# Optimization experiments

Measured on AMD Instinct MI355X. Metric: run time of the kernel, lower is better.

The kernel has to match this reference:

```python
import jax, jax.numpy as jnp
import numpy as np

N = 50000      # nodes
E = 800000     # edges
IN = 128       # in_dim
EMB = 32       # emb_dim
ED = 8         # edge_dim
L = 4          # num_layers
B = 64         # num graphs in batch
OUT = 10       # out_dim
EPS = 1e-5


def setup_inputs() -> dict:
    key = jax.random.key(0)
    ks = jax.random.split(key, 16)
    f32 = jnp.float32
    def nrm(k, shape, scale):
        return jax.random.normal(k, shape, dtype=f32) * scale
    inp = {}
    inp['x'] = nrm(ks[0], (N, IN), 1.0)
    inp['edge_index'] = jax.random.randint(ks[1], (2, E), 0, N)
    inp['edge_attr'] = nrm(ks[2], (E, ED), 1.0)
    inp['batch'] = jnp.sort(jax.random.randint(ks[3], (N,), 0, B))
    # lin_in
    inp['lin_in_w'] = nrm(ks[4], (IN, EMB), 0.05)
    inp['lin_in_b'] = jnp.zeros((EMB,), f32)
    # per-layer message MLP: Linear(2e+ed->e), BN, ReLU, Linear(e->e), BN, ReLU
    inp['msg_w1'] = nrm(ks[5], (L, 2 * EMB + ED, EMB), 0.1)
    inp['msg_b1'] = jnp.zeros((L, EMB), f32)
    inp['msg_g1'] = jnp.ones((L, EMB), f32)
    inp['msg_be1'] = jnp.zeros((L, EMB), f32)
    inp['msg_w2'] = nrm(ks[6], (L, EMB, EMB), 0.1)
    inp['msg_b2'] = jnp.zeros((L, EMB), f32)
    inp['msg_g2'] = jnp.ones((L, EMB), f32)
    inp['msg_be2'] = jnp.zeros((L, EMB), f32)
    # per-layer update MLP: Linear(2e->e), BN, ReLU, Linear(e->e), BN, ReLU
    inp['upd_w1'] = nrm(ks[7], (L, 2 * EMB, EMB), 0.1)
    inp['upd_b1'] = jnp.zeros((L, EMB), f32)
    inp['upd_g1'] = jnp.ones((L, EMB), f32)
    inp['upd_be1'] = jnp.zeros((L, EMB), f32)
    inp['upd_w2'] = nrm(ks[8], (L, EMB, EMB), 0.1)
    inp['upd_b2'] = jnp.zeros((L, EMB), f32)
    inp['upd_g2'] = jnp.ones((L, EMB), f32)
    inp['upd_be2'] = jnp.zeros((L, EMB), f32)
    # lin_pred
    inp['pred_w'] = nrm(ks[9], (EMB, OUT), 0.1)
    inp['pred_b'] = jnp.zeros((OUT,), f32)
    return inp


def _bn(x, g, b):
    # BatchNorm1d in training mode: batch stats over dim 0 (biased variance)
    mu = jnp.mean(x, axis=0)
    var = jnp.mean(jnp.square(x - mu), axis=0)
    return (x - mu) * jax.lax.rsqrt(var + EPS) * g + b


def reference(x, edge_attr, lin_in_w, lin_in_b,
              msg_w1, msg_b1, msg_g1, msg_be1, msg_w2, msg_b2, msg_g2, msg_be2,
              upd_w1, upd_b1, upd_g1, upd_be1, upd_w2, upd_b2, upd_g2, upd_be2,
              pred_w, pred_b, edge_index, batch):
    src = edge_index[0]  # h_j source nodes
    dst = edge_index[1]  # h_i target nodes (aggregation index)
    h = x @ lin_in_w + lin_in_b  # [N, EMB]
    for i in range(L):
        # message: gather + concat + MLP(BN,ReLU)x2 over edges
        msg_in = jnp.concatenate([h[dst], h[src], edge_attr], axis=-1)  # [E, 2e+ed]
        m = jax.nn.relu(_bn(msg_in @ msg_w1[i] + msg_b1[i], msg_g1[i], msg_be1[i]))
        m = jax.nn.relu(_bn(m @ msg_w2[i] + msg_b2[i], msg_g2[i], msg_be2[i]))
        # aggregate: scatter-add by destination
        aggr = jax.ops.segment_sum(m, dst, num_segments=N)  # [N, EMB]
        # update: concat + MLP(BN,ReLU)x2
        u = jnp.concatenate([h, aggr], axis=-1)  # [N, 2e]
        u = jax.nn.relu(_bn(u @ upd_w1[i] + upd_b1[i], upd_g1[i], upd_be1[i]))
        u = jax.nn.relu(_bn(u @ upd_w2[i] + upd_b2[i], upd_g2[i], upd_be2[i]))
        h = u + h  # residual in MPNNModel.get_embeddings
    # global mean pool
    sums = jax.ops.segment_sum(h, batch, num_segments=B)
    counts = jax.ops.segment_sum(jnp.ones((N,), h.dtype), batch, num_segments=B)
    h_graph = sums / jnp.maximum(counts, 1.0)[:, None]
    return h_graph @ pred_w + pred_b  # [B, OUT]
```

## Files before the change

kernel.cpp:

```cpp
#include <hip/hip_runtime.h>
#include <cstddef>

#define N_NODES 50000
#define N_EDGES 800000
#define IN_DIM  128
#define EMB     32
#define ED      8
#define NLAYERS 4
#define NB      64
#define OUTD    10
#define EPS_BN  1e-5f

#define EDGE_GRID 3125
#define NODE_GRID 196
#define NODE4_GRID 782
#define AU_GRID   6250
#define MSG1_EPT  2
#define MSG1_GRID 1563
#define NT16      50000
#define NTILE_N   3125
#define LIN_GRID  782
#define MSG2_TPW  16
#define MSG2_GRID 782

#define SREP 4

typedef short bf16x8 __attribute__((ext_vector_type(8)));
typedef float f32x4  __attribute__((ext_vector_type(4)));


__device__ __forceinline__ unsigned short f2bf(float x) {
  union { float f; unsigned u; } v; v.f = x;
  unsigned b = v.u + 0x7FFFu + ((v.u >> 16) & 1u);
  return (unsigned short)(b >> 16);
}
__device__ __forceinline__ float bf2f(unsigned short s) {
  union { unsigned u; float f; } v; v.u = ((unsigned)s) << 16;
  return v.f;
}

__device__ __forceinline__ void coef_from_stats(const float* __restrict__ stats_stage,
                                                const float* __restrict__ g,
                                                const float* __restrict__ be,
                                                float inv_count, float* __restrict__ cf) {
  if (threadIdx.x < EMB) {
    const int c = threadIdx.x;
    float s = 0.f, ss = 0.f;
#pragma unroll
    for (int r = 0; r < SREP; ++r) {
      s  += stats_stage[r*64 + c];
      ss += stats_stage[r*64 + EMB + c];
    }
    const float mu  = s * inv_count;
    const float var = ss * inv_count - mu*mu;
    const float a = g[c] * rsqrtf(var + EPS_BN);
    cf[c] = a;
    cf[EMB + c] = fmaf(-mu, a, be[c]);
  }
  __syncthreads();
}

__device__ __forceinline__ void block_stats_atomic(const float ts[EMB], const float tss[EMB],
                                                   float* __restrict__ stats_stage) {
  __shared__ float sred[256];
  const int lane = threadIdx.x & 63;
  const int wid  = threadIdx.x >> 6;
#pragma unroll
  for (int c = 0; c < EMB; ++c) {
    float a = ts[c];
    float q = tss[c];
#pragma unroll
    for (int o = 32; o > 0; o >>= 1) {
      a += __shfl_down(a, o, 64);
      q += __shfl_down(q, o, 64);
    }
    if (lane == 0) { sred[wid*64 + c] = a; sred[wid*64 + EMB + c] = q; }
  }
  __syncthreads();
  if (threadIdx.x < 64) {
    const float v = sred[threadIdx.x] + sred[64 + threadIdx.x] +
                    sred[128 + threadIdx.x] + sred[192 + threadIdx.x];
    atomicAdd(stats_stage + ((blockIdx.x & (SREP-1)) << 6) + threadIdx.x, v);
  }
}

__device__ __forceinline__ void wave_stats_atomic(float ts[8], float tss[8],
                                                  float* __restrict__ lds_s,
                                                  float* __restrict__ lds_q,
                                                  float* __restrict__ stats_stage) {
  const int lane = threadIdx.x & 63;
  const int wv   = threadIdx.x >> 6;
#pragma unroll
  for (int j = 0; j < 8; ++j) {
    float a = ts[j], b = tss[j];
#pragma unroll
    for (int o = 32; o > 0; o >>= 1) {
      a += __shfl_down(a, o, 64);
      b += __shfl_down(b, o, 64);
    }
    ts[j] = a; tss[j] = b;
  }
  if (lane == 0) {
#pragma unroll
    for (int j = 0; j < 8; ++j) {
      lds_s[wv*8 + j] = ts[j];
      lds_q[wv*8 + j] = tss[j];
    }
  }
  __syncthreads();
  if (threadIdx.x < 64) {
    const float v = (threadIdx.x < 32) ? lds_s[threadIdx.x] : lds_q[threadIdx.x - 32];
    atomicAdd(stats_stage + ((blockIdx.x & (SREP-1)) << 6) + threadIdx.x, v);
  }
}

__device__ __forceinline__ void mac8_f4(float acc[8], const float4 v, const float* wk) {
#pragma unroll
  for (int j = 0; j < 8; ++j) acc[j] = fmaf(v.x, wk[j], acc[j]);
#pragma unroll
  for (int j = 0; j < 8; ++j) acc[j] = fmaf(v.y, wk[EMB + j], acc[j]);
#pragma unroll
  for (int j = 0; j < 8; ++j) acc[j] = fmaf(v.z, wk[2*EMB + j], acc[j]);
#pragma unroll
  for (int j = 0; j < 8; ++j) acc[j] = fmaf(v.w, wk[3*EMB + j], acc[j]);
}

#define HSTRIDE 40

__global__ __launch_bounds__(256) void k_lin_in_pq(
    const float* __restrict__ x, const float* __restrict__ w, const float* __restrict__ b,
    const float* __restrict__ w1, const float* __restrict__ b1, const int* __restrict__ ei,
    float* __restrict__ h, unsigned short* __restrict__ p, unsigned short* __restrict__ q,
    int* __restrict__ cnt)
{
  __shared__ __align__(16) unsigned short lds_hb[4][16*HSTRIDE];
  __shared__ __align__(16) unsigned short lds_pq[4][16*HSTRIDE];
  const int lane = threadIdx.x & 63;
  const int wv   = threadIdx.x >> 6;
  const int n0i  = lane & 15;
  const int quad = lane >> 4;

  const int tile = blockIdx.x*4 + wv;
  if (tile < NTILE_N) {
    const int r0 = tile*16;
    bf16x8 BwL[4], BwH[4];
#pragma unroll
    for (int kb = 0; kb < 4; ++kb) {
#pragma unroll
      for (int j = 0; j < 8; ++j) {
        const int k = kb*32 + quad*8 + j;
        BwL[kb][j] = (short)f2bf(w[k*EMB + n0i]);
        BwH[kb][j] = (short)f2bf(w[k*EMB + 16 + n0i]);
      }
    }
    f32x4 accL = {0.f,0.f,0.f,0.f};
    f32x4 accH = {0.f,0.f,0.f,0.f};
#pragma unroll
    for (int kb = 0; kb < 4; ++kb) {
      const float4 xa = *(const float4*)(x + (size_t)(r0 + n0i)*IN_DIM + kb*32 + quad*8);
      const float4 xb = *(const float4*)(x + (size_t)(r0 + n0i)*IN_DIM + kb*32 + quad*8 + 4);
      bf16x8 A;
      A[0] = (short)f2bf(xa.x); A[1] = (short)f2bf(xa.y);
      A[2] = (short)f2bf(xa.z); A[3] = (short)f2bf(xa.w);
      A[4] = (short)f2bf(xb.x); A[5] = (short)f2bf(xb.y);
      A[6] = (short)f2bf(xb.z); A[7] = (short)f2bf(xb.w);
      accL = __builtin_amdgcn_mfma_f32_16x16x32_bf16(A, BwL[kb], accL, 0, 0, 0);
      accH = __builtin_amdgcn_mfma_f32_16x16x32_bf16(A, BwH[kb], accH, 0, 0, 0);
    }
    const float bL = b[n0i], bH = b[16 + n0i];
#pragma unroll
    for (int r = 0; r < 4; ++r) {
      const int row = quad*4 + r;
      const float vL = accL[r] + bL;
      const float vH = accH[r] + bH;
      h[(size_t)(r0 + row)*EMB + n0i]      = vL;
      h[(size_t)(r0 + row)*EMB + 16 + n0i] = vH;
      lds_hb[wv][row*HSTRIDE + n0i]      = f2bf(vL);
      lds_hb[wv][row*HSTRIDE + 16 + n0i] = f2bf(vH);
    }
    bf16x8 A2;
#pragma unroll
    for (int j = 0; j < 8; ++j)
      A2[j] = (short)lds_hb[wv][n0i*HSTRIDE + quad*8 + j];
    bf16x8 BpL, BpH, BqL, BqH;
#pragma unroll
    for (int j = 0; j < 8; ++j) {
      const int k = quad*8 + j;
      BpL[j] = (short)f2bf(w1[k*EMB + n0i]);
      BpH[j] = (short)f2bf(w1[k*EMB + 16 + n0i]);
      BqL[j] = (short)f2bf(w1[(EMB + k)*EMB + n0i]);
      BqH[j] = (short)f2bf(w1[(EMB + k)*EMB + 16 + n0i]);
    }
    const f32x4 z4 = {0.f,0.f,0.f,0.f};
    f32x4 pL = __builtin_amdgcn_mfma_f32_16x16x32_bf16(A2, BpL, z4, 0, 0, 0);
    f32x4 pH = __builtin_amdgcn_mfma_f32_16x16x32_bf16(A2, BpH, z4, 0, 0, 0);
    f32x4 qL = __builtin_amdgcn_mfma_f32_16x16x32_bf16(A2, BqL, z4, 0, 0, 0);
    f32x4 qH = __builtin_amdgcn_mfma_f32_16x16x32_bf16(A2, BqH, z4, 0, 0, 0);
    const float b1L = b1[n0i], b1H = b1[16 + n0i];
#pragma unroll
    for (int r = 0; r < 4; ++r) {
      const int row = quad*4 + r;
      lds_pq[wv][row*HSTRIDE + n0i]      = f2bf(pL[r] + b1L);
      lds_pq[wv][row*HSTRIDE + 16 + n0i] = f2bf(pH[r] + b1H);
    }
    {
      const int row2 = lane >> 2;
      const int c8   = (lane & 3)*8;
      const uint4 ov = *(const uint4*)&lds_pq[wv][row2*HSTRIDE + c8];
      *(uint4*)(p + (size_t)(r0 + row2)*EMB + c8) = ov;
    }
#pragma unroll
    for (int r = 0; r < 4; ++r) {
      const int row = quad*4 + r;
      lds_pq[wv][row*HSTRIDE + n0i]      = f2bf(qL[r]);
      lds_pq[wv][row*HSTRIDE + 16 + n0i] = f2bf(qH[r]);
    }
    {
      const int row2 = lane >> 2;
      const int c8   = (lane & 3)*8;
      const uint4 ov = *(const uint4*)&lds_pq[wv][row2*HSTRIDE + c8];
      *(uint4*)(q + (size_t)(r0 + row2)*EMB + c8) = ov;
    }
  }
  for (int e = blockIdx.x*256 + threadIdx.x; e < N_EDGES; e += gridDim.x*256)
    atomicAdd(&cnt[ei[N_EDGES + e]], 1);
}

__global__ __launch_bounds__(256) void k_scan_a(const int* __restrict__ cnt,
                                                int* __restrict__ row_ptr, int* __restrict__ bsum) {
  __shared__ int s[256];
  const int gid = blockIdx.x*256 + threadIdx.x;
  const int v = (gid < N_NODES) ? cnt[gid] : 0;
  s[threadIdx.x] = v;
  __syncthreads();
  for (int o = 1; o < 256; o <<= 1) {
    const int t = (threadIdx.x >= o) ? s[threadIdx.x - o] : 0;
    __syncthreads();
    s[threadIdx.x] += t;
    __syncthreads();
  }
  if (gid < N_NODES) row_ptr[gid] = s[threadIdx.x] - v;
  if (threadIdx.x == 255) bsum[blockIdx.x] = s[255];
}

__global__ __launch_bounds__(256) void k_scan_bc(int* __restrict__ row_ptr,
                                                 const int* __restrict__ bsum) {
  __shared__ int s[256];
  const int t = threadIdx.x;
  const int v = (t < NODE_GRID) ? bsum[t] : 0;
  s[t] = v;
  __syncthreads();
  for (int o = 1; o < 256; o <<= 1) {
    const int tt = (t >= o) ? s[t - o] : 0;
    __syncthreads();
    s[t] += tt;
    __syncthreads();
  }
  const int off = (blockIdx.x == 0) ? 0 : s[blockIdx.x - 1];
  const int gid = blockIdx.x*256 + t;
  if (gid < N_NODES) row_ptr[gid] += off;
  if (blockIdx.x == 0 && t == 0) row_ptr[N_NODES] = N_EDGES;
}

__global__ __launch_bounds__(256) void k_place_scatter(
    const int* __restrict__ ei, const float* __restrict__ ea,
    const int* __restrict__ row_ptr, int* __restrict__ cnt2,
    int* __restrict__ src_perm, int* __restrict__ dst_perm,
    unsigned short* __restrict__ ea_perm)
{
  const int e = blockIdx.x*256 + threadIdx.x;
  const int d = ei[N_EDGES + e];
  const int pos = row_ptr[d] + atomicAdd(&cnt2[d], 1);
  src_perm[pos] = ei[e];
  dst_perm[pos] = d;
  const float4 v0 = ((const float4*)(ea + (size_t)e*ED))[0];
  const float4 v1 = ((const float4*)(ea + (size_t)e*ED))[1];
  const float ev[8] = {v0.x, v0.y, v0.z, v0.w, v1.x, v1.y, v1.z, v1.w};
  unsigned u[4];
#pragma unroll
  for (int j = 0; j < 4; ++j)
    u[j] = (unsigned)f2bf(ev[2*j]) | ((unsigned)f2bf(ev[2*j+1]) << 16);
  uint4 o; o.x = u[0]; o.y = u[1]; o.z = u[2]; o.w = u[3];
  *(uint4*)(ea_perm + (size_t)pos*ED) = o;
}


__global__ __launch_bounds__(256) void k_msg1(
    const unsigned short* __restrict__ pb, const unsigned short* __restrict__ qb,
    const int* __restrict__ src_perm, const int* __restrict__ dst_perm,
    const unsigned short* __restrict__ ea_perm,
    const float* __restrict__ w1b,
    unsigned short* __restrict__ y, float* __restrict__ stats)
{
  float ts[EMB], tss[EMB];
#pragma unroll
  for (int c = 0; c < EMB; ++c) { ts[c] = 0.f; tss[c] = 0.f; }
  const int base = blockIdx.x*(256*MSG1_EPT) + threadIdx.x;
  for (int it = 0; it < MSG1_EPT; ++it) {
    const int i = base + it*256;
    if (i >= N_EDGES) break;
    const int dst = dst_perm[i];
    const int src = src_perm[i];
    float acc[EMB];
    const uint4* pd = (const uint4*)(pb + (size_t)dst*EMB);
    const uint4* qs = (const uint4*)(qb + (size_t)src*EMB);
#pragma unroll
    for (int j4 = 0; j4 < 4; ++j4) {
      const uint4 a = pd[j4];
      const uint4 b = qs[j4];
      const unsigned ua[4] = {a.x, a.y, a.z, a.w};
      const unsigned ub[4] = {b.x, b.y, b.z, b.w};
#pragma unroll
      for (int t = 0; t < 4; ++t) {
        acc[j4*8 + 2*t]   = bf2f((unsigned short)(ua[t] & 0xFFFFu)) +
                            bf2f((unsigned short)(ub[t] & 0xFFFFu));
        acc[j4*8 + 2*t+1] = bf2f((unsigned short)(ua[t] >> 16)) +
                            bf2f((unsigned short)(ub[t] >> 16));
      }
    }
    const uint4 eraw = *(const uint4*)(ea_perm + (size_t)i*ED);
    const unsigned ue[4] = {eraw.x, eraw.y, eraw.z, eraw.w};
    float ev[8];
#pragma unroll
    for (int t = 0; t < 4; ++t) {
      ev[2*t]   = bf2f((unsigned short)(ue[t] & 0xFFFFu));
      ev[2*t+1] = bf2f((unsigned short)(ue[t] >> 16));
    }
#pragma unroll
    for (int k = 0; k < 8; ++k) {
      const float* wk = w1b + k*EMB;
#pragma unroll
      for (int c = 0; c < EMB; ++c) acc[c] = fmaf(ev[k], wk[c], acc[c]);
    }
    unsigned short us[EMB];
#pragma unroll
    for (int c = 0; c < EMB; ++c) us[c] = f2bf(acc[c]);
    unsigned u[16];
#pragma unroll
    for (int j = 0; j < 16; ++j)
      u[j] = (unsigned)us[2*j] | ((unsigned)us[2*j+1] << 16);
    uint4* dp = (uint4*)(y + (size_t)i*EMB);
#pragma unroll
    for (int j = 0; j < 4; ++j) {
      uint4 o; o.x = u[4*j]; o.y = u[4*j+1]; o.z = u[4*j+2]; o.w = u[4*j+3];
      dp[j] = o;
    }
#pragma unroll
    for (int c = 0; c < EMB; ++c) {
      const float v = bf2f(us[c]);
      ts[c] += v;
      tss[c] = fmaf(v, v, tss[c]);
    }
  }
  block_stats_atomic(ts, tss, stats);
}

__global__ __launch_bounds__(256) void k_msg2(
    unsigned short* __restrict__ y,
    const float* __restrict__ stats1, const float* __restrict__ g1, const float* __restrict__ be1,
    const float* __restrict__ w2, const float* __restrict__ b2,
    float* __restrict__ stats2)
{
  __shared__ __align__(16) unsigned short lds_t[4][16*32];
  __shared__ float lds_s[4][32], lds_q[4][32];
  __shared__ float cf[64];

  coef_from_stats(stats1, g1, be1, 1.0f/(float)N_EDGES, cf);

  const int lane = threadIdx.x & 63;
  const int wid  = threadIdx.x >> 6;
  const int n0 = lane & 15;
  const int kb = lane >> 4;

  bf16x8 Blo, Bhi;
#pragma unroll
  for (int j = 0; j < 8; ++j) {
    Blo[j] = (short)f2bf(w2[(kb*8 + j)*EMB + n0]);
    Bhi[j] = (short)f2bf(w2[(kb*8 + j)*EMB + 16 + n0]);
  }
  float a1[8], c1[8];
#pragma unroll
  for (int j = 0; j < 8; ++j) {
    a1[j] = cf[kb*8 + j];
    c1[j] = cf[EMB + kb*8 + j];
  }
  const float b2c0 = b2[n0], b2c1 = b2[16 + n0];

  float ts[8], tss[8];
#pragma unroll
  for (int j = 0; j < 8; ++j) { ts[j] = 0.f; tss[j] = 0.f; }

  const int tile0 = blockIdx.x * (MSG2_TPW*4);
  for (int t = 0; t < MSG2_TPW; ++t) {
    const int tile = tile0 + t*4 + wid;
    if (tile >= NT16) break;
    const size_t e0 = (size_t)tile * 16;

    const uint4 araw = *(const uint4*)(y + (e0 + n0)*EMB + kb*8);
    unsigned int ua[4] = {araw.x, araw.y, araw.z, araw.w};
    bf16x8 A;
#pragma unroll
    for (int j = 0; j < 4; ++j) {
      float v0 = bf2f((unsigned short)(ua[j] & 0xFFFFu));
      float v1 = bf2f((unsigned short)(ua[j] >> 16));
      v0 = fmaxf(fmaf(a1[2*j],   v0, c1[2*j]),   0.f);
      v1 = fmaxf(fmaf(a1[2*j+1], v1, c1[2*j+1]), 0.f);
      A[2*j]   = (short)f2bf(v0);
      A[2*j+1] = (short)f2bf(v1);
    }

    f32x4 acc0 = {0.f, 0.f, 0.f, 0.f};
    f32x4 acc1 = {0.f, 0.f, 0.f, 0.f};
    acc0 = __builtin_amdgcn_mfma_f32_16x16x32_bf16(A, Blo, acc0, 0, 0, 0);
    acc1 = __builtin_amdgcn_mfma_f32_16x16x32_bf16(A, Bhi, acc1, 0, 0, 0);

#pragma unroll
    for (int r = 0; r < 4; ++r) {
      const int row = kb*4 + r;
      lds_t[wid][row*32 + n0]      = f2bf(acc0[r] + b2c0);
      lds_t[wid][row*32 + 16 + n0] = f2bf(acc1[r] + b2c1);
    }
    const uint4 orow = *(const uint4*)&lds_t[wid][(lane>>2)*32 + (lane&3)*8];
    *(uint4*)(y + (e0 + (lane>>2))*EMB + (lane&3)*8) = orow;

    unsigned int uo[4] = {orow.x, orow.y, orow.z, orow.w};
#pragma unroll
    for (int j = 0; j < 4; ++j) {
      const float v0 = bf2f((unsigned short)(uo[j] & 0xFFFFu));
      const float v1 = bf2f((unsigned short)(uo[j] >> 16));
      ts[2*j]   += v0;  tss[2*j]   = fmaf(v0, v0, tss[2*j]);
      ts[2*j+1] += v1;  tss[2*j+1] = fmaf(v1, v1, tss[2*j+1]);
    }
  }

#pragma unroll
  for (int j = 0; j < 8; ++j) {
    float s = ts[j], qq = tss[j];
#pragma unroll
    for (int o = 4; o < 64; o <<= 1) {
      s  += __shfl_xor(s, o, 64);
      qq += __shfl_xor(qq, o, 64);
    }
    ts[j] = s; tss[j] = qq;
  }
  if (lane < 4) {
#pragma unroll
    for (int j = 0; j < 8; ++j) {
      lds_s[wid][lane*8 + j] = ts[j];
      lds_q[wid][lane*8 + j] = tss[j];
    }
  }
  __syncthreads();
  if (threadIdx.x < 64) {
    const int c = threadIdx.x & 31;
    const int kind = threadIdx.x >> 5;
    float v = 0.f;
#pragma unroll
    for (int wq = 0; wq < 4; ++wq)
      v += kind ? lds_q[wq][c] : lds_s[wq][c];
    atomicAdd(stats2 + ((blockIdx.x & (SREP-1)) << 6) + kind*32 + c, v);
  }
}

__global__ __launch_bounds__(256) void k_aggr_upd1(
    const unsigned short* __restrict__ y, const int* __restrict__ row_ptr,
    const float* __restrict__ h,
    const float* __restrict__ stats1, const float* __restrict__ g2, const float* __restrict__ be2,
    const float* __restrict__ uw1, const float* __restrict__ ub1,
    float* __restrict__ z, float* __restrict__ stats2)
{
  __shared__ float cf[64];
  __shared__ float lh[8][32];
  __shared__ float la[8][32];
  __shared__ float rs[4][32], rq[4][32];
  coef_from_stats(stats1, g2, be2, 1.0f/(float)N_EDGES, cf);

  const int g = threadIdx.x >> 5;
  const int l = threadIdx.x & 31;
  const int n = blockIdx.x*8 + g;

  lh[g][l] = h[(size_t)n*EMB + l];

  const int rof = l >> 4;
  const int cp  = l & 15;
  const float a0 = cf[2*cp],     b0 = cf[EMB + 2*cp];
  const float a1 = cf[2*cp + 1], b1 = cf[EMB + 2*cp + 1];
  const int lo = row_ptr[n], hi = row_ptr[n+1];
  float s0 = 0.f, s1 = 0.f;
  for (int i = lo + rof; i < hi; i += 2) {
    const unsigned u = *(const unsigned*)(y + (size_t)i*EMB + 2*cp);
    const float v0 = bf2f((unsigned short)(u & 0xFFFFu));
    const float v1 = bf2f((unsigned short)(u >> 16));
    s0 += fmaxf(fmaf(a0, v0, b0), 0.f);
    s1 += fmaxf(fmaf(a1, v1, b1), 0.f);
  }
  s0 += __shfl_xor(s0, 16, 64);
  s1 += __shfl_xor(s1, 16, 64);
  if (rof == 0) { la[g][2*cp] = s0; la[g][2*cp + 1] = s1; }
  __syncthreads();

  float acc = ub1[l];
#pragma unroll
  for (int k = 0; k < EMB; ++k) acc = fmaf(lh[g][k], uw1[k*EMB + l], acc);
#pragma unroll
  for (int k = 0; k < EMB; ++k) acc = fmaf(la[g][k], uw1[(EMB + k)*EMB + l], acc);
  z[(size_t)n*EMB + l] = acc;

  const float sq = acc*acc;
  const float a2 = acc + __shfl_down(acc, 32, 64);
  const float q2 = sq  + __shfl_down(sq,  32, 64);
  const int wv = threadIdx.x >> 6;
  if ((threadIdx.x & 63) < 32) { rs[wv][l] = a2; rq[wv][l] = q2; }
  __syncthreads();
  if (threadIdx.x < 64) {
    const int c = threadIdx.x & 31;
    const int kind = threadIdx.x >> 5;
    float v = 0.f;
#pragma unroll
    for (int wq = 0; wq < 4; ++wq)
      v += kind ? rq[wq][c] : rs[wq][c];
    atomicAdd(stats2 + ((blockIdx.x & (SREP-1)) << 6) + kind*32 + c, v);
  }
}

__global__ __launch_bounds__(256) void k_upd2(
    float* __restrict__ z,
    const float* __restrict__ stats1, const float* __restrict__ g1, const float* __restrict__ be1,
    const float* __restrict__ w, const float* __restrict__ b,
    float* __restrict__ stats2)
{
  __shared__ float cf[64];
  __shared__ float lds_s[32], lds_q[32];
  coef_from_stats(stats1, g1, be1, 1.0f/(float)N_NODES, cf);

  const int lane = threadIdx.x & 63;
  const int wv   = threadIdx.x >> 6;
  const int n  = blockIdx.x*64 + lane;
  const int c0 = wv*8;
  float acc[8];
#pragma unroll
  for (int j = 0; j < 8; ++j) acc[j] = 0.f;
  if (n < N_NODES) {
#pragma unroll
    for (int j = 0; j < 8; ++j) acc[j] = b[c0 + j];
    const float4* zp = (const float4*)(z + (size_t)n*EMB);
#pragma unroll
    for (int k4 = 0; k4 < 8; ++k4) {
      const float4 v = zp[k4];
      const float mv[4] = {v.x, v.y, v.z, v.w};
#pragma unroll
      for (int t = 0; t < 4; ++t) {
        const int k = 4*k4 + t;
        const float m = fmaxf(fmaf(cf[k], mv[t], cf[EMB + k]), 0.f);
        const float* wk = w + k*EMB + c0;
#pragma unroll
        for (int j = 0; j < 8; ++j) acc[j] = fmaf(m, wk[j], acc[j]);
      }
    }
  }
  float ts[8], tss[8];
#pragma unroll
  for (int j = 0; j < 8; ++j) { ts[j] = acc[j]; tss[j] = acc[j]*acc[j]; }
  wave_stats_atomic(ts, tss, lds_s, lds_q, stats2);
  if (n < N_NODES) {
    float4 o0, o1;
    o0.x = acc[0]; o0.y = acc[1]; o0.z = acc[2]; o0.w = acc[3];
    o1.x = acc[4]; o1.y = acc[5]; o1.z = acc[6]; o1.w = acc[7];
    *(float4*)(z + (size_t)n*EMB + c0)     = o0;
    *(float4*)(z + (size_t)n*EMB + c0 + 4) = o1;
  }
}

__global__ __launch_bounds__(256) void k_resid_pq(
    float* __restrict__ h, const float* __restrict__ z,
    const float* __restrict__ stats, const float* __restrict__ g, const float* __restrict__ be,
    const float* __restrict__ w1_next, const float* __restrict__ b1_next,
    unsigned short* __restrict__ p, unsigned short* __restrict__ q)
{
  __shared__ float cf[64];
  __shared__ float lds_h[64][33];
  coef_from_stats(stats, g, be, 1.0f/(float)N_NODES, cf);

  const int lane = threadIdx.x & 63;
  const int wv   = threadIdx.x >> 6;
  const int n  = blockIdx.x*64 + lane;
  const int c0 = wv*8;
  if (n < N_NODES) {
    const float4* zp = (const float4*)(z + (size_t)n*EMB + c0);
    float4* hp = (float4*)(h + (size_t)n*EMB + c0);
    float hn[8];
    const float4 z0 = zp[0], z1 = zp[1];
    const float4 h0 = hp[0], h1 = hp[1];
    const float zv[8] = {z0.x, z0.y, z0.z, z0.w, z1.x, z1.y, z1.z, z1.w};
    const float hv[8] = {h0.x, h0.y, h0.z, h0.w, h1.x, h1.y, h1.z, h1.w};
#pragma unroll
    for (int j = 0; j < 8; ++j) {
      const int k = c0 + j;
      hn[j] = hv[j] + fmaxf(fmaf(cf[k], zv[j], cf[EMB + k]), 0.f);
      lds_h[lane][k] = hn[j];
    }
    float4 o0, o1;
    o0.x = hn[0]; o0.y = hn[1]; o0.z = hn[2]; o0.w = hn[3];
    o1.x = hn[4]; o1.y = hn[5]; o1.z = hn[6]; o1.w = hn[7];
    hp[0] = o0; hp[1] = o1;
  }
  __syncthreads();
  if (n < N_NODES && w1_next) {
    float ap[8], aq[8];
#pragma unroll
    for (int j = 0; j < 8; ++j) { ap[j] = b1_next[c0 + j]; aq[j] = 0.f; }
#pragma unroll
    for (int k = 0; k < EMB; ++k) {
      const float hvv = lds_h[lane][k];
      const float* wp = w1_next + k*EMB + c0;
      const float* wq = w1_next + (EMB + k)*EMB + c0;
#pragma unroll
      for (int j = 0; j < 8; ++j) ap[j] = fmaf(hvv, wp[j], ap[j]);
#pragma unroll
      for (int j = 0; j < 8; ++j) aq[j] = fmaf(hvv, wq[j], aq[j]);
    }
    unsigned up[4], uq[4];
#pragma unroll
    for (int j = 0; j < 4; ++j) {
      up[j] = (unsigned)f2bf(ap[2*j]) | ((unsigned)f2bf(ap[2*j+1]) << 16);
      uq[j] = (unsigned)f2bf(aq[2*j]) | ((unsigned)f2bf(aq[2*j+1]) << 16);
    }
    uint4 op; op.x = up[0]; op.y = up[1]; op.z = up[2]; op.w = up[3];
    uint4 oq; oq.x = uq[0]; oq.y = uq[1]; oq.z = uq[2]; oq.w = uq[3];
    *(uint4*)(p + (size_t)n*EMB + c0) = op;
    *(uint4*)(q + (size_t)n*EMB + c0) = oq;
  }
}

__global__ void k_pool(const float* __restrict__ h, const int* __restrict__ batch,
                       const float* __restrict__ pw, const float* __restrict__ pb,
                       float* __restrict__ out)
{
  __shared__ float sred[256];
  __shared__ float hg[EMB];
  const int b = blockIdx.x;
  int lo = 0, hi = N_NODES;
  while (lo < hi) { int m = (lo + hi) >> 1; if (batch[m] < b) lo = m + 1; else hi = m; }
  const int start = lo;
  hi = N_NODES;
  while (lo < hi) { int m = (lo + hi) >> 1; if (batch[m] < b + 1) lo = m + 1; else hi = m; }
  const int end = lo;

  const int c = threadIdx.x & (EMB-1);
  const int r = threadIdx.x >> 5;
  float s = 0.f;
  for (int n = start + r; n < end; n += 8) s += h[(size_t)n*EMB + c];
  sred[threadIdx.x] = s;
  __syncthreads();
  if (threadIdx.x < EMB) {
    float tot = 0.f;
#pragma unroll
    for (int r2 = 0; r2 < 8; ++r2) tot += sred[r2*EMB + threadIdx.x];
    const float cnt = (float)(end - start);
    hg[threadIdx.x] = tot / fmaxf(cnt, 1.f);
  }
  __syncthreads();
  if (threadIdx.x < OUTD) {
    float acc = pb[threadIdx.x];
#pragma unroll
    for (int cc = 0; cc < EMB; ++cc) acc = fmaf(hg[cc], pw[cc*OUTD + threadIdx.x], acc);
    out[b*OUTD + threadIdx.x] = acc;
  }
}


extern "C" void kernel_launch(void* const* d_in, const int* in_sizes, int n_in,
                              void* d_out, int out_size, void* d_ws, size_t ws_size,
                              hipStream_t stream) {
  const float* x        = (const float*)d_in[0];
  const int*   ei       = (const int*)  d_in[1];
  const float* ea       = (const float*)d_in[2];
  const int*   batch    = (const int*)  d_in[3];
  const float* lin_in_w = (const float*)d_in[4];
  const float* lin_in_b = (const float*)d_in[5];
  const float* msg_w1   = (const float*)d_in[6];
  const float* msg_b1   = (const float*)d_in[7];
  const float* msg_g1   = (const float*)d_in[8];
  const float* msg_be1  = (const float*)d_in[9];
  const float* msg_w2   = (const float*)d_in[10];
  const float* msg_b2   = (const float*)d_in[11];
  const float* msg_g2   = (const float*)d_in[12];
  const float* msg_be2  = (const float*)d_in[13];
  const float* upd_w1   = (const float*)d_in[14];
  const float* upd_b1   = (const float*)d_in[15];
  const float* upd_g1   = (const float*)d_in[16];
  const float* upd_be1  = (const float*)d_in[17];
  const float* upd_w2   = (const float*)d_in[18];
  const float* upd_b2   = (const float*)d_in[19];
  const float* upd_g2   = (const float*)d_in[20];
  const float* upd_be2  = (const float*)d_in[21];
  const float* pred_w   = (const float*)d_in[22];
  const float* pred_b   = (const float*)d_in[23];
  float* out = (float*)d_out;

  char* wsb = (char*)d_ws;
  unsigned short* y  = (unsigned short*)wsb;
  unsigned short* eap= (unsigned short*)(wsb + (size_t)N_EDGES*EMB*2);
  unsigned short* p  = eap + (size_t)N_EDGES*ED;
  unsigned short* q  = p + (size_t)N_NODES*EMB;
  float* h       = (float*)(q + (size_t)N_NODES*EMB);
  float* z       = h + (size_t)N_NODES*EMB;
  float* stats   = z + (size_t)N_NODES*EMB;
  int*   cnt     = (int*)(stats + 16*SREP*64);
  int*   cnt2    = cnt + N_NODES;
  int*   row_ptr = cnt2 + N_NODES;
  int*   bsum    = row_ptr + N_NODES + 1;
  int*   src_perm= bsum + 256;
  int*   dst_perm= src_perm + N_EDGES;
  const size_t need = ((size_t)((char*)(dst_perm + N_EDGES) - wsb));
  if (ws_size < need) return;

  hipMemsetAsync(stats, 0, (16*SREP*64 + 2*N_NODES)*sizeof(float), stream);

  k_lin_in_pq<<<LIN_GRID, 256, 0, stream>>>(x, lin_in_w, lin_in_b, msg_w1, msg_b1, ei,
                                            h, p, q, cnt);
  k_scan_a<<<NODE_GRID, 256, 0, stream>>>(cnt, row_ptr, bsum);
  k_scan_bc<<<NODE_GRID, 256, 0, stream>>>(row_ptr, bsum);
  k_place_scatter<<<EDGE_GRID, 256, 0, stream>>>(ei, ea, row_ptr, cnt2,
                                                 src_perm, dst_perm, eap);

  for (int l = 0; l < NLAYERS; ++l) {
    const int st = l*4;
    const float* w1  = msg_w1 + (size_t)l*(2*EMB+ED)*EMB;
    const float* w1b = w1 + (size_t)2*EMB*EMB;
    const float* w2  = msg_w2 + (size_t)l*EMB*EMB;
    const float* uw1 = upd_w1 + (size_t)l*(2*EMB)*EMB;
    const float* uw2 = upd_w2 + (size_t)l*EMB*EMB;
    const float* w1_next = (l+1 < NLAYERS) ? msg_w1 + (size_t)(l+1)*(2*EMB+ED)*EMB : nullptr;
    const float* b1_next = (l+1 < NLAYERS) ? msg_b1 + (size_t)(l+1)*EMB : nullptr;

    k_msg1<<<MSG1_GRID, 256, 0, stream>>>(p, q, src_perm, dst_perm, eap,
                                          w1b, y, stats + (size_t)st*SREP*64);
    k_msg2<<<MSG2_GRID, 256, 0, stream>>>(y, stats + (size_t)st*SREP*64,
                                          msg_g1 + l*EMB, msg_be1 + l*EMB,
                                          w2, msg_b2 + l*EMB, stats + (size_t)(st+1)*SREP*64);
    k_aggr_upd1<<<AU_GRID, 256, 0, stream>>>(y, row_ptr, h,
                                             stats + (size_t)(st+1)*SREP*64,
                                             msg_g2 + l*EMB, msg_be2 + l*EMB,
                                             uw1, upd_b1 + l*EMB,
                                             z, stats + (size_t)(st+2)*SREP*64);
    k_upd2<<<NODE4_GRID, 256, 0, stream>>>(z, stats + (size_t)(st+2)*SREP*64,
                                           upd_g1 + l*EMB, upd_be1 + l*EMB,
                                           uw2, upd_b2 + l*EMB, stats + (size_t)(st+3)*SREP*64);
    k_resid_pq<<<NODE4_GRID, 256, 0, stream>>>(h, z, stats + (size_t)(st+3)*SREP*64,
                                               upd_g2 + l*EMB, upd_be2 + l*EMB,
                                               w1_next, b1_next, p, q);
  }

  k_pool<<<NB, 256, 0, stream>>>(h, batch, pred_w, pred_b, out);
}
```

Baseline: 895.3 us.

## Pack edge records and split msg1 channels across thread pairs

The separate src_perm, dst_perm and bf16 edge-attribute arrays are merged into one 24-byte interleaved record per sorted edge, so msg1 fetches its indices and attributes from a single location. msg1 now has each pair of threads share an edge, with each thread computing 16 of the 32 output channels for two edges, and the grid grows to one block per 256 edges. This cuts per-thread registers and raises parallelism and memory-level concurrency for the gathers. In exchange, the record layout uses 8-byte accesses with a stride of three, and the stats reduction changes to a half-width shuffle scheme.

```diff
diff --git a/kernel.cpp b/kernel.cpp
--- a/kernel.cpp
+++ b/kernel.cpp
@@ -15,8 +15,6 @@
 #define NODE_GRID 196
 #define NODE4_GRID 782
 #define AU_GRID   6250
-#define MSG1_EPT  2
-#define MSG1_GRID 1563
 #define NT16      50000
 #define NTILE_N   3125
 #define LIN_GRID  782
@@ -60,30 +58,6 @@
   __syncthreads();
 }
 
-__device__ __forceinline__ void block_stats_atomic(const float ts[EMB], const float tss[EMB],
-                                                   float* __restrict__ stats_stage) {
-  __shared__ float sred[256];
-  const int lane = threadIdx.x & 63;
-  const int wid  = threadIdx.x >> 6;
-#pragma unroll
-  for (int c = 0; c < EMB; ++c) {
-    float a = ts[c];
-    float q = tss[c];
-#pragma unroll
-    for (int o = 32; o > 0; o >>= 1) {
-      a += __shfl_down(a, o, 64);
-      q += __shfl_down(q, o, 64);
-    }
-    if (lane == 0) { sred[wid*64 + c] = a; sred[wid*64 + EMB + c] = q; }
-  }
-  __syncthreads();
-  if (threadIdx.x < 64) {
-    const float v = sred[threadIdx.x] + sred[64 + threadIdx.x] +
-                    sred[128 + threadIdx.x] + sred[192 + threadIdx.x];
-    atomicAdd(stats_stage + ((blockIdx.x & (SREP-1)) << 6) + threadIdx.x, v);
-  }
-}
-
 __device__ __forceinline__ void wave_stats_atomic(float ts[8], float tss[8],
                                                   float* __restrict__ lds_s,
                                                   float* __restrict__ lds_q,
@@ -114,15 +88,31 @@
   }
 }
 
-__device__ __forceinline__ void mac8_f4(float acc[8], const float4 v, const float* wk) {
-#pragma unroll
-  for (int j = 0; j < 8; ++j) acc[j] = fmaf(v.x, wk[j], acc[j]);
-#pragma unroll
-  for (int j = 0; j < 8; ++j) acc[j] = fmaf(v.y, wk[EMB + j], acc[j]);
-#pragma unroll
-  for (int j = 0; j < 8; ++j) acc[j] = fmaf(v.z, wk[2*EMB + j], acc[j]);
-#pragma unroll
-  for (int j = 0; j < 8; ++j) acc[j] = fmaf(v.w, wk[3*EMB + j], acc[j]);
+__device__ __forceinline__ void half_stats_atomic(const float ts[16], const float tss[16],
+                                                  float* __restrict__ stats_stage) {
+  __shared__ float s_s[4][32], s_q[4][32];
+  const int lane = threadIdx.x & 63;
+  const int wid  = threadIdx.x >> 6;
+#pragma unroll
+  for (int j = 0; j < 16; ++j) {
+    float a = ts[j], q = tss[j];
+#pragma unroll
+    for (int o = 32; o >= 2; o >>= 1) {
+      a += __shfl_down(a, o, 64);
+      q += __shfl_down(q, o, 64);
+    }
+    if (lane < 2) { s_s[wid][lane*16 + j] = a; s_q[wid][lane*16 + j] = q; }
+  }
+  __syncthreads();
+  if (threadIdx.x < 64) {
+    const int c = threadIdx.x & 31;
+    const int kind = threadIdx.x >> 5;
+    float v = 0.f;
+#pragma unroll
+    for (int wq = 0; wq < 4; ++wq)
+      v += kind ? s_q[wq][c] : s_s[wq][c];
+    atomicAdd(stats_stage + ((blockIdx.x & (SREP-1)) << 6) + kind*32 + c, v);
+  }
 }
 
 #define HSTRIDE 40
@@ -265,14 +255,12 @@
 __global__ __launch_bounds__(256) void k_place_scatter(
     const int* __restrict__ ei, const float* __restrict__ ea,
     const int* __restrict__ row_ptr, int* __restrict__ cnt2,
-    int* __restrict__ src_perm, int* __restrict__ dst_perm,
-    unsigned short* __restrict__ ea_perm)
+    uint2* __restrict__ rec)
 {
   const int e = blockIdx.x*256 + threadIdx.x;
+  const int s = ei[e];
   const int d = ei[N_EDGES + e];
   const int pos = row_ptr[d] + atomicAdd(&cnt2[d], 1);
-  src_perm[pos] = ei[e];
-  dst_perm[pos] = d;
   const float4 v0 = ((const float4*)(ea + (size_t)e*ED))[0];
   const float4 v1 = ((const float4*)(ea + (size_t)e*ED))[1];
   const float ev[8] = {v0.x, v0.y, v0.z, v0.w, v1.x, v1.y, v1.z, v1.w};
@@ -280,79 +268,103 @@
 #pragma unroll
   for (int j = 0; j < 4; ++j)
     u[j] = (unsigned)f2bf(ev[2*j]) | ((unsigned)f2bf(ev[2*j+1]) << 16);
-  uint4 o; o.x = u[0]; o.y = u[1]; o.z = u[2]; o.w = u[3];
-  *(uint4*)(ea_perm + (size_t)pos*ED) = o;
-}
-
+  uint2* rp = rec + (size_t)pos*3;
+  rp[0] = make_uint2((unsigned)s, (unsigned)d);
+  rp[1] = make_uint2(u[0], u[1]);
+  rp[2] = make_uint2(u[2], u[3]);
+}
+
+
+__device__ __forceinline__ void msg1_edge(const uint4 Pa, const uint4 Pb,
+                                          const uint4 Qa, const uint4 Qb,
+                                          const uint2 rb, const uint2 rc,
+                                          const float* __restrict__ wh,
+                                          float acc[16])
+{
+  const unsigned pw[8] = {Pa.x,Pa.y,Pa.z,Pa.w,Pb.x,Pb.y,Pb.z,Pb.w};
+  const unsigned qw[8] = {Qa.x,Qa.y,Qa.z,Qa.w,Qb.x,Qb.y,Qb.z,Qb.w};
+#pragma unroll
+  for (int t = 0; t < 8; ++t) {
+    acc[2*t]   = bf2f((unsigned short)(pw[t] & 0xFFFFu)) +
+                 bf2f((unsigned short)(qw[t] & 0xFFFFu));
+    acc[2*t+1] = bf2f((unsigned short)(pw[t] >> 16)) +
+                 bf2f((unsigned short)(qw[t] >> 16));
+  }
+  const unsigned ew[4] = {rb.x, rb.y, rc.x, rc.y};
+  float ev[8];
+#pragma unroll
+  for (int t = 0; t < 4; ++t) {
+    ev[2*t]   = bf2f((unsigned short)(ew[t] & 0xFFFFu));
+    ev[2*t+1] = bf2f((unsigned short)(ew[t] >> 16));
+  }
+#pragma unroll
+  for (int k = 0; k < 8; ++k) {
+    const float* wk = wh + k*EMB;
+#pragma unroll
+    for (int j = 0; j < 16; ++j) acc[j] = fmaf(ev[k], wk[j], acc[j]);
+  }
+}
+
+__device__ __forceinline__ void msg1_store_stats(const float acc[16],
+                                                 unsigned short* __restrict__ dst,
+                                                 float ts[16], float tss[16])
+{
+  unsigned u[8];
+#pragma unroll
+  for (int j = 0; j < 8; ++j) {
+    const unsigned short l0 = f2bf(acc[2*j]);
+    const unsigned short h0 = f2bf(acc[2*j+1]);
+    u[j] = (unsigned)l0 | ((unsigned)h0 << 16);
+    const float v0 = bf2f(l0), v1 = bf2f(h0);
+    ts[2*j]   += v0; tss[2*j]   = fmaf(v0, v0, tss[2*j]);
+    ts[2*j+1] += v1; tss[2*j+1] = fmaf(v1, v1, tss[2*j+1]);
+  }
+  uint4 o0; o0.x = u[0]; o0.y = u[1]; o0.z = u[2]; o0.w = u[3];
+  uint4 o1; o1.x = u[4]; o1.y = u[5]; o1.z = u[6]; o1.w = u[7];
+  ((uint4*)dst)[0] = o0;
+  ((uint4*)dst)[1] = o1;
+}
 
 __global__ __launch_bounds__(256) void k_msg1(
     const unsigned short* __restrict__ pb, const unsigned short* __restrict__ qb,
-    const int* __restrict__ src_perm, const int* __restrict__ dst_perm,
-    const unsigned short* __restrict__ ea_perm,
-    const float* __restrict__ w1b,
+    const uint2* __restrict__ rec, const float* __restrict__ w1b,
     unsigned short* __restrict__ y, float* __restrict__ stats)
 {
-  float ts[EMB], tss[EMB];
-#pragma unroll
-  for (int c = 0; c < EMB; ++c) { ts[c] = 0.f; tss[c] = 0.f; }
-  const int base = blockIdx.x*(256*MSG1_EPT) + threadIdx.x;
-  for (int it = 0; it < MSG1_EPT; ++it) {
-    const int i = base + it*256;
-    if (i >= N_EDGES) break;
-    const int dst = dst_perm[i];
-    const int src = src_perm[i];
-    float acc[EMB];
-    const uint4* pd = (const uint4*)(pb + (size_t)dst*EMB);
-    const uint4* qs = (const uint4*)(qb + (size_t)src*EMB);
-#pragma unroll
-    for (int j4 = 0; j4 < 4; ++j4) {
-      const uint4 a = pd[j4];
-      const uint4 b = qs[j4];
-      const unsigned ua[4] = {a.x, a.y, a.z, a.w};
-      const unsigned ub[4] = {b.x, b.y, b.z, b.w};
-#pragma unroll
-      for (int t = 0; t < 4; ++t) {
-        acc[j4*8 + 2*t]   = bf2f((unsigned short)(ua[t] & 0xFFFFu)) +
-                            bf2f((unsigned short)(ub[t] & 0xFFFFu));
-        acc[j4*8 + 2*t+1] = bf2f((unsigned short)(ua[t] >> 16)) +
-                            bf2f((unsigned short)(ub[t] >> 16));
-      }
-    }
-    const uint4 eraw = *(const uint4*)(ea_perm + (size_t)i*ED);
-    const unsigned ue[4] = {eraw.x, eraw.y, eraw.z, eraw.w};
-    float ev[8];
-#pragma unroll
-    for (int t = 0; t < 4; ++t) {
-      ev[2*t]   = bf2f((unsigned short)(ue[t] & 0xFFFFu));
-      ev[2*t+1] = bf2f((unsigned short)(ue[t] >> 16));
-    }
-#pragma unroll
-    for (int k = 0; k < 8; ++k) {
-      const float* wk = w1b + k*EMB;
-#pragma unroll
-      for (int c = 0; c < EMB; ++c) acc[c] = fmaf(ev[k], wk[c], acc[c]);
-    }
-    unsigned short us[EMB];
-#pragma unroll
-    for (int c = 0; c < EMB; ++c) us[c] = f2bf(acc[c]);
-    unsigned u[16];
-#pragma unroll
-    for (int j = 0; j < 16; ++j)
-      u[j] = (unsigned)us[2*j] | ((unsigned)us[2*j+1] << 16);
-    uint4* dp = (uint4*)(y + (size_t)i*EMB);
-#pragma unroll
-    for (int j = 0; j < 4; ++j) {
-      uint4 o; o.x = u[4*j]; o.y = u[4*j+1]; o.z = u[4*j+2]; o.w = u[4*j+3];
-      dp[j] = o;
-    }
-#pragma unroll
-    for (int c = 0; c < EMB; ++c) {
-      const float v = bf2f(us[c]);
-      ts[c] += v;
-      tss[c] = fmaf(v, v, tss[c]);
-    }
-  }
-  block_stats_atomic(ts, tss, stats);
+  const int t    = threadIdx.x;
+  const int half = t & 1;
+  const int eh   = t >> 1;
+  const int e0   = blockIdx.x*256 + eh;
+  const int e1   = e0 + 128;
+
+  const uint2 r0a = rec[(size_t)e0*3];
+  const uint2 r0b = rec[(size_t)e0*3 + 1];
+  const uint2 r0c = rec[(size_t)e0*3 + 2];
+  const uint2 r1a = rec[(size_t)e1*3];
+  const uint2 r1b = rec[(size_t)e1*3 + 1];
+  const uint2 r1c = rec[(size_t)e1*3 + 2];
+
+  const uint4* p0 = (const uint4*)(pb + (size_t)r0a.y * EMB) + half*2;
+  const uint4* q0 = (const uint4*)(qb + (size_t)r0a.x * EMB) + half*2;
+  const uint4* p1 = (const uint4*)(pb + (size_t)r1a.y * EMB) + half*2;
+  const uint4* q1 = (const uint4*)(qb + (size_t)r1a.x * EMB) + half*2;
+  const uint4 P0a = p0[0], P0b = p0[1];
+  const uint4 Q0a = q0[0], Q0b = q0[1];
+  const uint4 P1a = p1[0], P1b = p1[1];
+  const uint4 Q1a = q1[0], Q1b = q1[1];
+
+  const float* wh = w1b + half*16;
+
+  float ts[16], tss[16];
+#pragma unroll
+  for (int j = 0; j < 16; ++j) { ts[j] = 0.f; tss[j] = 0.f; }
+
+  float acc[16];
+  msg1_edge(P0a, P0b, Q0a, Q0b, r0b, r0c, wh, acc);
+  msg1_store_stats(acc, y + (size_t)e0*EMB + half*16, ts, tss);
+  msg1_edge(P1a, P1b, Q1a, Q1b, r1b, r1c, wh, acc);
+  msg1_store_stats(acc, y + (size_t)e1*EMB + half*16, ts, tss);
+
+  half_stats_atomic(ts, tss, stats);
 }
 
 __global__ __launch_bounds__(256) void k_msg2(
@@ -700,8 +712,8 @@
 
   char* wsb = (char*)d_ws;
   unsigned short* y  = (unsigned short*)wsb;
-  unsigned short* eap= (unsigned short*)(wsb + (size_t)N_EDGES*EMB*2);
-  unsigned short* p  = eap + (size_t)N_EDGES*ED;
+  uint2* rec = (uint2*)(wsb + (size_t)N_EDGES*EMB*2);
+  unsigned short* p  = (unsigned short*)(rec + (size_t)N_EDGES*3);
   unsigned short* q  = p + (size_t)N_NODES*EMB;
   float* h       = (float*)(q + (size_t)N_NODES*EMB);
   float* z       = h + (size_t)N_NODES*EMB;
@@ -710,9 +722,7 @@
   int*   cnt2    = cnt + N_NODES;
   int*   row_ptr = cnt2 + N_NODES;
   int*   bsum    = row_ptr + N_NODES + 1;
-  int*   src_perm= bsum + 256;
-  int*   dst_perm= src_perm + N_EDGES;
-  const size_t need = ((size_t)((char*)(dst_perm + N_EDGES) - wsb));
+  const size_t need = ((size_t)((char*)(bsum + 256) - wsb));
   if (ws_size < need) return;
 
   hipMemsetAsync(stats, 0, (16*SREP*64 + 2*N_NODES)*sizeof(float), stream);
@@ -721,8 +731,7 @@
                                             h, p, q, cnt);
   k_scan_a<<<NODE_GRID, 256, 0, stream>>>(cnt, row_ptr, bsum);
   k_scan_bc<<<NODE_GRID, 256, 0, stream>>>(row_ptr, bsum);
-  k_place_scatter<<<EDGE_GRID, 256, 0, stream>>>(ei, ea, row_ptr, cnt2,
-                                                 src_perm, dst_perm, eap);
+  k_place_scatter<<<EDGE_GRID, 256, 0, stream>>>(ei, ea, row_ptr, cnt2, rec);
 
   for (int l = 0; l < NLAYERS; ++l) {
     const int st = l*4;
@@ -734,8 +743,7 @@
     const float* w1_next = (l+1 < NLAYERS) ? msg_w1 + (size_t)(l+1)*(2*EMB+ED)*EMB : nullptr;
     const float* b1_next = (l+1 < NLAYERS) ? msg_b1 + (size_t)(l+1)*EMB : nullptr;
 
-    k_msg1<<<MSG1_GRID, 256, 0, stream>>>(p, q, src_perm, dst_perm, eap,
-                                          w1b, y, stats + (size_t)st*SREP*64);
+    k_msg1<<<EDGE_GRID, 256, 0, stream>>>(p, q, rec, w1b, y, stats + (size_t)st*SREP*64);
     k_msg2<<<MSG2_GRID, 256, 0, stream>>>(y, stats + (size_t)st*SREP*64,
                                           msg_g1 + l*EMB, msg_be1 + l*EMB,
                                           w2, msg_b2 + l*EMB, stats + (size_t)(st+1)*SREP*64);
```

Result: no change. 905.3 us (+1.1%).
